# Kernel tuning notes

Hardware: AMD Instinct MI355X
Metric: run time of the kernel (lower is better)

## Reference

```python
import jax, jax.numpy as jnp
import numpy as np

T, B, DIM, N = 2048, 8, 1024, 64

def setup_inputs() -> dict:
    key = jax.random.key(0)
    ks = jax.random.split(key, 6)
    scale = 1.0 / np.sqrt(DIM)  # xavier-ish for Linear(dim, n_state)
    return {
        "x": jax.random.normal(ks[0], (T, B, DIM), dtype=jnp.float32),
        "S0": jnp.zeros((B, N, N), dtype=jnp.float32),
        "W_k": jax.random.normal(ks[1], (N, DIM), dtype=jnp.float32) * scale,
        "W_v": jax.random.normal(ks[2], (N, DIM), dtype=jnp.float32) * scale,
        "W_q": jax.random.normal(ks[3], (N, DIM), dtype=jnp.float32) * scale,
        "W_alpha": jax.random.normal(ks[4], (N, DIM), dtype=jnp.float32) * scale,
        "b_alpha": jnp.full((N,), 2.0, dtype=jnp.float32),
        "d_g": jnp.full((N,), 0.5, dtype=jnp.float32),
        "b_g": jnp.zeros((N,), dtype=jnp.float32),
    }

def reference(x, S0, W_k, W_v, W_q, W_alpha, b_alpha, d_g, b_g):
    # Precompute all projections: [T, B, N]
    k_all = jnp.einsum('tbd,nd->tbn', x, W_k)
    v_all = jnp.einsum('tbd,nd->tbn', x, W_v)
    q_all = jnp.einsum('tbd,nd->tbn', x, W_q)
    alpha_all = jax.nn.sigmoid(jnp.einsum('tbd,nd->tbn', x, W_alpha) + b_alpha)

    def step(S, inp):
        k, v, q, alpha = inp  # each [B, N]
        retrieved = jnp.einsum('bij,bj->bi', S, k)          # S @ k
        g = jax.nn.sigmoid(d_g * retrieved + b_g)
        v_gated = v * g
        outer_vk = jnp.einsum('bi,bj->bij', v_gated, k)
        S = alpha[..., None] * S + (1.0 - alpha[..., None]) * outer_vk
        out = jnp.einsum('bij,bj->bi', S, q)                # S @ q
        out = out * jax.nn.silu(out)                        # self-gate
        return S, out

    S_final, output = jax.lax.scan(step, S0, (k_all, v_all, q_all, alpha_all))
    return output, S_final
```

## Files before the change

### kernel.cpp

```cpp
#include <hip/hip_runtime.h>

#define TT 2048
#define BB 8
#define DD 1024
#define NN 64
#define C64 64
#define NC2 (TT / C64)

typedef __attribute__((ext_vector_type(8))) short bfrag;
typedef __attribute__((ext_vector_type(4))) float f32x4;
typedef __attribute__((ext_vector_type(8))) unsigned short ushort8;

__device__ __forceinline__ float rcp_(float x) { return __builtin_amdgcn_rcpf(x); }
__device__ __forceinline__ float exp2_(float x) {
#if __has_builtin(__builtin_amdgcn_exp2f)
    return __builtin_amdgcn_exp2f(x);
#else
    return exp2f(x);
#endif
}
__device__ __forceinline__ float sigmoidf_(float x) {
    return rcp_(1.0f + __expf(-x));
}
__device__ __forceinline__ float bcastlane(float x, int l) {
    return __int_as_float(__builtin_amdgcn_readlane(__float_as_int(x), l));
}

template <int CTRL, int RM>
__device__ __forceinline__ float dpp_mul1(float x) {
    int v = __builtin_amdgcn_update_dpp(
        0x3f800000, __float_as_int(x), CTRL, RM, 0xF, false);
    return x * __int_as_float(v);
}
__device__ __forceinline__ float prefix_mul64(float x) {
    x = dpp_mul1<0x111, 0xF>(x);
    x = dpp_mul1<0x112, 0xF>(x);
    x = dpp_mul1<0x114, 0xF>(x);
    x = dpp_mul1<0x118, 0xF>(x);
    x = dpp_mul1<0x142, 0xA>(x);
    x = dpp_mul1<0x143, 0xC>(x);
    return x;
}

__device__ __forceinline__ unsigned short cvt_bf16(float f) {
    unsigned int u = __float_as_uint(f);
    return (unsigned short)((u + 0x7FFF + ((u >> 16) & 1)) >> 16);
}

__device__ __forceinline__ void gll16(const float* g, float* l) {
    __builtin_amdgcn_global_load_lds(
        (const __attribute__((address_space(1))) void*)g,
        (__attribute__((address_space(3))) void*)l, 16, 0, 0);
}

__global__ __launch_bounds__(256) void wcvt_kernel(
    const float* __restrict__ W0, const float* __restrict__ W1,
    const float* __restrict__ W2, const float* __restrict__ W3,
    unsigned short* __restrict__ Wb)
{
    const int i = blockIdx.x * 256 + threadIdx.x;
    const int o = i * 8;
    const int col = o & 31;
    const int row = (o >> 5) & 63;
    const int kt  = (o >> 11) & 31;
    const int mat = o >> 16;
    const float* __restrict__ W = (mat == 0) ? W0 : (mat == 1) ? W1
                                 : (mat == 2) ? W2 : W3;
    const float* src = &W[(size_t)row * DD + kt * 32 + col];
    const float4 a = *(const float4*)src;
    const float4 b = *(const float4*)(src + 4);
    ushort8 r;
    r[0] = cvt_bf16(a.x); r[1] = cvt_bf16(a.y);
    r[2] = cvt_bf16(a.z); r[3] = cvt_bf16(a.w);
    r[4] = cvt_bf16(b.x); r[5] = cvt_bf16(b.y);
    r[6] = cvt_bf16(b.z); r[7] = cvt_bf16(b.w);
    *(ushort8*)&Wb[o] = r;
}

__global__ __launch_bounds__(256) void proj_fused_kernel(
    const float* __restrict__ x, const unsigned short* __restrict__ Wb,
    const float* __restrict__ b_alpha,
    float* __restrict__ O0, float* __restrict__ O1,
    float* __restrict__ O2, float* __restrict__ O3)
{
    const int m0   = blockIdx.x * 64;
    const int tid  = threadIdx.x;
    const int lane = tid & 63;
    const int wave = tid >> 6;
    const int ln   = lane & 15;
    const int q8   = (lane >> 4) * 8;

    __shared__ unsigned short As[64][40];
    __shared__ unsigned short Bs[4][64][40];

    f32x4 acc[4][4] = {};

    const int arow = tid >> 2;
    const int aseg = (tid & 3) * 8;

    float4 pa[2];
    ushort8 pw[4];
    {
        const float* ap = &x[(size_t)(m0 + arow) * DD + aseg];
        pa[0] = *(const float4*)ap;
        pa[1] = *(const float4*)(ap + 4);
        const ushort8* wp = (const ushort8*)&Wb[((size_t)(wave * 32 + 0) * 64 + lane) * 32];
        #pragma unroll
        for (int j = 0; j < 4; j++) pw[j] = wp[j];
    }

    for (int k0 = 0; k0 < DD; k0 += 32) {
        __syncthreads();
        {
            unsigned short t8[8];
            const float* pf = (const float*)pa;
            #pragma unroll
            for (int j = 0; j < 8; j++) t8[j] = cvt_bf16(pf[j]);
            *(ushort8*)&As[arow][aseg] = *(ushort8*)&t8[0];
            #pragma unroll
            for (int j = 0; j < 4; j++)
                *(ushort8*)&Bs[wave][lane][8 * j] = pw[j];
        }
        if (k0 + 32 < DD) {
            const int kt = (k0 >> 5) + 1;
            const float* ap = &x[(size_t)(m0 + arow) * DD + k0 + 32 + aseg];
            pa[0] = *(const float4*)ap;
            pa[1] = *(const float4*)(ap + 4);
            const ushort8* wp = (const ushort8*)&Wb[((size_t)(wave * 32 + kt) * 64 + lane) * 32];
            #pragma unroll
            for (int j = 0; j < 4; j++) pw[j] = wp[j];
        }
        __syncthreads();

        const bfrag af = *(const bfrag*)&As[wave * 16 + ln][q8];
        #pragma unroll
        for (int mat = 0; mat < 4; mat++) {
            bfrag bf[4];
            #pragma unroll
            for (int nt = 0; nt < 4; nt++)
                bf[nt] = *(const bfrag*)&Bs[mat][nt * 16 + ln][q8];
            #pragma unroll
            for (int nt = 0; nt < 4; nt++)
                acc[mat][nt] = __builtin_amdgcn_mfma_f32_16x16x32_bf16(
                    af, bf[nt], acc[mat][nt], 0, 0, 0);
        }
    }

    #pragma unroll
    for (int mat = 0; mat < 4; mat++) {
        float* __restrict__ C = (mat == 0) ? O0 : (mat == 1) ? O1
                               : (mat == 2) ? O2 : O3;
        #pragma unroll
        for (int nt = 0; nt < 4; nt++) {
            const int col = nt * 16 + ln;
            const float ba = (mat == 3) ? b_alpha[col] : 0.0f;
            #pragma unroll
            for (int r = 0; r < 4; r++) {
                const int row = m0 + wave * 16 + (lane >> 4) * 4 + r;
                float v = acc[mat][nt][r];
                if (mat == 3) v = sigmoidf_(v + ba);
                C[(size_t)row * NN + col] = v;
            }
        }
    }
}

__global__ __launch_bounds__(256) void gram_kernel(
    const float* __restrict__ k_all, const float* __restrict__ q_all,
    float* __restrict__ gkq)
{
    const int c  = blockIdx.x;
    const int b  = blockIdx.y;
    const int t0 = c * C64;
    const int tid = threadIdx.x;

    __shared__ __align__(16) float Ks[64][68];
    __shared__ __align__(16) float Qs[64][68];

    {
        const int r = tid >> 2, sg = (tid & 3) * 16;
        const float* kp = &k_all[(size_t)(t0 + r) * (BB * NN) + b * NN + sg];
        const float* qp = &q_all[(size_t)(t0 + r) * (BB * NN) + b * NN + sg];
        #pragma unroll
        for (int j = 0; j < 4; ++j) {
            *(float4*)&Ks[r][sg + 4 * j] = *(const float4*)(kp + 4 * j);
            *(float4*)&Qs[r][sg + 4 * j] = *(const float4*)(qp + 4 * j);
        }
    }
    __syncthreads();

    const int ti = tid >> 4, tj = tid & 15;
    float g[4][4] = {}, kq[4][4] = {};
    #pragma unroll
    for (int c4 = 0; c4 < 16; ++c4) {
        float4 ka[4], kb[4], qb[4];
        #pragma unroll
        for (int r = 0; r < 4; ++r) {
            ka[r] = *(const float4*)&Ks[4 * ti + r][c4 * 4];
            kb[r] = *(const float4*)&Ks[4 * tj + r][c4 * 4];
            qb[r] = *(const float4*)&Qs[4 * tj + r][c4 * 4];
        }
        #pragma unroll
        for (int r = 0; r < 4; ++r)
            #pragma unroll
            for (int q = 0; q < 4; ++q) {
                g[r][q]  = fmaf(ka[r].x, kb[q].x, g[r][q]);
                g[r][q]  = fmaf(ka[r].y, kb[q].y, g[r][q]);
                g[r][q]  = fmaf(ka[r].z, kb[q].z, g[r][q]);
                g[r][q]  = fmaf(ka[r].w, kb[q].w, g[r][q]);
                kq[r][q] = fmaf(ka[r].x, qb[q].x, kq[r][q]);
                kq[r][q] = fmaf(ka[r].y, qb[q].y, kq[r][q]);
                kq[r][q] = fmaf(ka[r].z, qb[q].z, kq[r][q]);
                kq[r][q] = fmaf(ka[r].w, qb[q].w, kq[r][q]);
            }
    }

    float* base = gkq + (size_t)(b * NC2 + c) * 64 * 128;
    #pragma unroll
    for (int r = 0; r < 4; ++r) {
        #pragma unroll
        for (int q = 0; q < 4; ++q) {
            const int t   = 4 * tj + q;
            const int pos = ((ti ^ (t & 15)) << 2) + r;
            base[t * 128 + pos]      = g[r][q];
            base[t * 128 + 64 + pos] = kq[r][q];
        }
    }
}

__global__ __launch_bounds__(128, 1) void scan_kernel(
    const float* __restrict__ gkq,
    const float* __restrict__ k_all, const float* __restrict__ q_all,
    const float* __restrict__ a_all, const float* __restrict__ v_all,
    const float* __restrict__ S0,
    const float* __restrict__ d_g, const float* __restrict__ b_g,
    float* __restrict__ out, float* __restrict__ S_final)
{
    const int b    = blockIdx.x;
    const int rg   = blockIdx.y;
    const int tid  = threadIdx.x;
    const int lane = tid & 63;
    const int wave = tid >> 6;
    const int row  = rg * 2 + wave;

    __shared__ __align__(16) float gT[2][64 * 128];
    __shared__ __align__(16) float Kl[2][64 * 64];
    __shared__ __align__(16) float Ql[2][64 * 64];
    __shared__ __align__(16) float sbuf[2][64];

    float S = S0[((size_t)b * NN + row) * NN + lane];
    const float L2E  = 1.4426950408889634f;
    const float ndg2 = -d_g[row] * L2E;
    const float nbg2 = -b_g[row] * L2E;

    const float* gkq_b = gkq + (size_t)b * NC2 * 64 * 128;

    const int s_loc = lane >> 4;
    const int gr    = lane & 15;

    auto stage = [&](int c, int db) {
        const float* src = gkq_b + (size_t)c * 64 * 128;
        #pragma unroll
        for (int j = 0; j < 16; ++j) {
            const int off = (wave * 32 + 2 * j) * 128;
            gll16(src + off + lane * 4, &gT[db][off]);
        }
        #pragma unroll
        for (int j = 0; j < 8; ++j) {
            const int r0 = wave * 32 + 4 * j;
            const int s  = r0 + s_loc;
            const int gg = gr ^ (s & 15);
            const size_t goff = ((size_t)(c * C64 + s) * BB + b) * NN + gg * 4;
            gll16(k_all + goff, &Kl[db][r0 * 64]);
            gll16(q_all + goff, &Ql[db][r0 * 64]);
        }
    };

    float a_nx, v_nx;
    auto aw_load = [&](int c) {
        const size_t goff = ((size_t)(c * C64 + lane) * BB + b) * NN + row;
        a_nx = a_all[goff];
        v_nx = v_all[goff];
    };

    stage(0, 0);
    aw_load(0);

    for (int c = 0; c < NC2; ++c) {
        const int db = c & 1;
        const float ac = a_nx;
        const float wc = (1.0f - a_nx) * v_nx;
        __syncthreads();
        if (c + 1 < NC2) { aw_load(c + 1); stage(c + 1, db ^ 1); }

        const float P  = prefix_mul64(ac);
        const float Pm = P / ac;
        const float u  = wc * rcp_(P);

        sbuf[wave][lane] = S;
        const float* Kb = &Kl[db][0];
        const float* Qb = &Ql[db][0];
        float4 ha = {0.f, 0.f, 0.f, 0.f};
        float4 hb = {0.f, 0.f, 0.f, 0.f};
        #pragma unroll
        for (int g4 = 0; g4 < 16; ++g4) {
            const int idx = lane * 64 + ((g4 ^ gr) << 2);
            float4 kv = *(const float4*)&Kb[idx];
            float4 qv = *(const float4*)&Qb[idx];
            float4 sv = *(const float4*)&sbuf[wave][g4 << 2];
            ha.x = fmaf(kv.x, sv.x, ha.x); ha.y = fmaf(kv.y, sv.y, ha.y);
            ha.z = fmaf(kv.z, sv.z, ha.z); ha.w = fmaf(kv.w, sv.w, ha.w);
            hb.x = fmaf(qv.x, sv.x, hb.x); hb.y = fmaf(qv.y, sv.y, hb.y);
            hb.z = fmaf(qv.z, sv.z, hb.z); hb.w = fmaf(qv.w, sv.w, hb.w);
        }
        const float h  = (ha.x + ha.y) + (ha.z + ha.w);
        const float hq = (hb.x + hb.y) + (hb.z + hb.w);
        const float e1 = ndg2 * Pm;
        const float e0 = fmaf(e1, h, nbg2);

        const float* gt = &gT[db][0];
        const int rowbase = lane * 128;

        float A = 0.f, Bacc = 0.f, Bl = 0.f, chl = 0.f;

        float4 ga0, ga1, qa0, qa1, gb0, gb1, qb0, qb1;

#define LOADBLK(G0, G1, Q0, Q1, blk) do {                                   \
        const int j0_ = ((2 * (blk)) ^ gr) << 2;                            \
        const int j1_ = ((2 * (blk) + 1) ^ gr) << 2;                        \
        G0 = *(const float4*)&gt[rowbase + j0_];                            \
        G1 = *(const float4*)&gt[rowbase + j1_];                            \
        Q0 = *(const float4*)&gt[rowbase + 64 + j0_];                       \
        Q1 = *(const float4*)&gt[rowbase + 64 + j1_];                       \
    } while (0)

#define STEP1(ss, gv, qv) do {                                              \
        const float sg_  = rcp_(1.0f + exp2_(fmaf(e1, A, e0)));             \
        const float s2_  = sg_ * u;                                         \
        const float chs_ = bcastlane(s2_, (ss));                            \
        A    = fmaf(chs_, (gv), A);                                         \
        Bacc = fmaf(chs_, (qv), Bacc);                                      \
        if (lane == (ss)) { Bl = Bacc; chl = chs_; }                        \
    } while (0)

#define STEP8(blk, G0, G1, Q0, Q1)                                          \
        STEP1(8 * (blk) + 0, G0.x, Q0.x); STEP1(8 * (blk) + 1, G0.y, Q0.y); \
        STEP1(8 * (blk) + 2, G0.z, Q0.z); STEP1(8 * (blk) + 3, G0.w, Q0.w); \
        STEP1(8 * (blk) + 4, G1.x, Q1.x); STEP1(8 * (blk) + 5, G1.y, Q1.y); \
        STEP1(8 * (blk) + 6, G1.z, Q1.z); STEP1(8 * (blk) + 7, G1.w, Q1.w);

        LOADBLK(ga0, ga1, qa0, qa1, 0);
        LOADBLK(gb0, gb1, qb0, qb1, 1);
        STEP8(0, ga0, ga1, qa0, qa1); LOADBLK(ga0, ga1, qa0, qa1, 2);
        STEP8(1, gb0, gb1, qb0, qb1); LOADBLK(gb0, gb1, qb0, qb1, 3);
        STEP8(2, ga0, ga1, qa0, qa1); LOADBLK(ga0, ga1, qa0, qa1, 4);
        STEP8(3, gb0, gb1, qb0, qb1); LOADBLK(gb0, gb1, qb0, qb1, 5);
        STEP8(4, ga0, ga1, qa0, qa1); LOADBLK(ga0, ga1, qa0, qa1, 6);
        STEP8(5, gb0, gb1, qb0, qb1); LOADBLK(gb0, gb1, qb0, qb1, 7);
        STEP8(6, ga0, ga1, qa0, qa1);
        STEP8(7, gb0, gb1, qb0, qb1);

#undef LOADBLK
#undef STEP1
#undef STEP8

        float Sa = 0.f;
        #pragma unroll
        for (int s = 0; s < 64; ++s) {
            const float chs = bcastlane(chl, s);
            const float kv  = Kb[s * 64 + (((lane >> 2) ^ (s & 15)) << 2) + (lane & 3)];
            Sa = fmaf(chs, kv, Sa);
        }

        const float o = P * (hq + Bl);
        const float y = o * o * rcp_(1.0f + exp2_(-o * L2E));
        out[((size_t)(c * C64 + lane) * BB + b) * NN + row] = y;
        const float Pl = bcastlane(P, 63);
        S = Pl * (S + Sa);
    }

    S_final[((size_t)b * NN + row) * NN + lane] = S;
}

extern "C" void kernel_launch(void* const* d_in, const int* in_sizes, int n_in,
                              void* d_out, int out_size, void* d_ws, size_t ws_size,
                              hipStream_t stream) {
    const float* x       = (const float*)d_in[0];
    const float* S0      = (const float*)d_in[1];
    const float* W_k     = (const float*)d_in[2];
    const float* W_v     = (const float*)d_in[3];
    const float* W_q     = (const float*)d_in[4];
    const float* W_alpha = (const float*)d_in[5];
    const float* b_alpha = (const float*)d_in[6];
    const float* d_g     = (const float*)d_in[7];
    const float* b_g     = (const float*)d_in[8];
    float* out = (float*)d_out;

    const size_t arr = (size_t)TT * BB * NN;
    float* ws    = (float*)d_ws;
    float* k_all = ws;
    float* v_all = ws + arr;
    float* q_all = ws + 2 * arr;
    float* a_all = ws + 3 * arr;
    float* gkq   = ws + 4 * arr;
    unsigned short* Wb = (unsigned short*)(ws + 6 * arr);

    wcvt_kernel<<<dim3(128), 256, 0, stream>>>(W_k, W_v, W_q, W_alpha, Wb);

    proj_fused_kernel<<<dim3(TT * BB / 64), 256, 0, stream>>>(
        x, Wb, b_alpha, k_all, v_all, q_all, a_all);

    gram_kernel<<<dim3(NC2, BB), 256, 0, stream>>>(k_all, q_all, gkq);

    scan_kernel<<<dim3(BB, 32), 128, 0, stream>>>(
        gkq, k_all, q_all, a_all, v_all, S0, d_g, b_g, out, out + arr);
}
```

Measured before the change: 319.9 us.

## Process four state rows per single-wave scan block with interleaved serial chains

```diff
diff --git a/kernel.cpp b/kernel.cpp
--- a/kernel.cpp
+++ b/kernel.cpp
@@ -228,7 +228,7 @@
     }
 }
 
-__global__ __launch_bounds__(128, 1) void scan_kernel(
+__global__ __launch_bounds__(64, 1) void scan_kernel(
     const float* __restrict__ gkq,
     const float* __restrict__ k_all, const float* __restrict__ q_all,
     const float* __restrict__ a_all, const float* __restrict__ v_all,
@@ -238,49 +238,52 @@
 {
     const int b    = blockIdx.x;
     const int rg   = blockIdx.y;
-    const int tid  = threadIdx.x;
-    const int lane = tid & 63;
-    const int wave = tid >> 6;
-    const int row  = rg * 2 + wave;
+    const int r0   = rg * 4;
+    const int lane = threadIdx.x;
+    const int gr    = lane & 15;
+    const int s_loc = lane >> 4;
 
     __shared__ __align__(16) float gT[2][64 * 128];
     __shared__ __align__(16) float Kl[2][64 * 64];
     __shared__ __align__(16) float Ql[2][64 * 64];
-    __shared__ __align__(16) float sbuf[2][64];
-
-    float S = S0[((size_t)b * NN + row) * NN + lane];
-    const float L2E  = 1.4426950408889634f;
-    const float ndg2 = -d_g[row] * L2E;
-    const float nbg2 = -b_g[row] * L2E;
+    __shared__ __align__(16) float sbuf[4][64];
+
+    const float L2E = 1.4426950408889634f;
+    const float4 dg4 = *(const float4*)&d_g[r0];
+    const float4 bg4 = *(const float4*)&b_g[r0];
+    float ndg2[4], nbg2[4], Sr[4];
+    #pragma unroll
+    for (int r = 0; r < 4; ++r) {
+        ndg2[r] = -((const float*)&dg4)[r] * L2E;
+        nbg2[r] = -((const float*)&bg4)[r] * L2E;
+        Sr[r]   = S0[((size_t)b * NN + r0 + r) * NN + lane];
+    }
 
     const float* gkq_b = gkq + (size_t)b * NC2 * 64 * 128;
-
-    const int s_loc = lane >> 4;
-    const int gr    = lane & 15;
 
     auto stage = [&](int c, int db) {
         const float* src = gkq_b + (size_t)c * 64 * 128;
         #pragma unroll
+        for (int j = 0; j < 32; ++j) {
+            const int off = (2 * j) * 128;
+            gll16(src + off + lane * 4, &gT[db][off]);
+        }
+        #pragma unroll
         for (int j = 0; j < 16; ++j) {
-            const int off = (wave * 32 + 2 * j) * 128;
-            gll16(src + off + lane * 4, &gT[db][off]);
-        }
-        #pragma unroll
-        for (int j = 0; j < 8; ++j) {
-            const int r0 = wave * 32 + 4 * j;
-            const int s  = r0 + s_loc;
+            const int rr = 4 * j;
+            const int s  = rr + s_loc;
             const int gg = gr ^ (s & 15);
             const size_t goff = ((size_t)(c * C64 + s) * BB + b) * NN + gg * 4;
-            gll16(k_all + goff, &Kl[db][r0 * 64]);
-            gll16(q_all + goff, &Ql[db][r0 * 64]);
+            gll16(k_all + goff, &Kl[db][rr * 64]);
+            gll16(q_all + goff, &Ql[db][rr * 64]);
         }
     };
 
-    float a_nx, v_nx;
+    float4 a_nx, v_nx;
     auto aw_load = [&](int c) {
-        const size_t goff = ((size_t)(c * C64 + lane) * BB + b) * NN + row;
-        a_nx = a_all[goff];
-        v_nx = v_all[goff];
+        const size_t goff = ((size_t)(c * C64 + lane) * BB + b) * NN + r0;
+        a_nx = *(const float4*)&a_all[goff];
+        v_nx = *(const float4*)&v_all[goff];
     };
 
     stage(0, 0);
@@ -288,66 +291,93 @@
 
     for (int c = 0; c < NC2; ++c) {
         const int db = c & 1;
-        const float ac = a_nx;
-        const float wc = (1.0f - a_nx) * v_nx;
+        float ac[4], wc[4];
+        #pragma unroll
+        for (int r = 0; r < 4; ++r) {
+            ac[r] = ((const float*)&a_nx)[r];
+            wc[r] = (1.0f - ac[r]) * ((const float*)&v_nx)[r];
+        }
         __syncthreads();
         if (c + 1 < NC2) { aw_load(c + 1); stage(c + 1, db ^ 1); }
 
-        const float P  = prefix_mul64(ac);
-        const float Pm = P / ac;
-        const float u  = wc * rcp_(P);
-
-        sbuf[wave][lane] = S;
+        float P[4], u[4], e1[4];
+        #pragma unroll
+        for (int r = 0; r < 4; ++r) {
+            P[r]  = prefix_mul64(ac[r]);
+            const float Pm = P[r] / ac[r];
+            u[r]  = wc[r] * rcp_(P[r]);
+            e1[r] = ndg2[r] * Pm;
+        }
+
+        #pragma unroll
+        for (int r = 0; r < 4; ++r) sbuf[r][lane] = Sr[r];
         const float* Kb = &Kl[db][0];
         const float* Qb = &Ql[db][0];
-        float4 ha = {0.f, 0.f, 0.f, 0.f};
-        float4 hb = {0.f, 0.f, 0.f, 0.f};
+        f32x4 hk[4] = {}, hqv[4] = {};
         #pragma unroll
         for (int g4 = 0; g4 < 16; ++g4) {
             const int idx = lane * 64 + ((g4 ^ gr) << 2);
-            float4 kv = *(const float4*)&Kb[idx];
-            float4 qv = *(const float4*)&Qb[idx];
-            float4 sv = *(const float4*)&sbuf[wave][g4 << 2];
-            ha.x = fmaf(kv.x, sv.x, ha.x); ha.y = fmaf(kv.y, sv.y, ha.y);
-            ha.z = fmaf(kv.z, sv.z, ha.z); ha.w = fmaf(kv.w, sv.w, ha.w);
-            hb.x = fmaf(qv.x, sv.x, hb.x); hb.y = fmaf(qv.y, sv.y, hb.y);
-            hb.z = fmaf(qv.z, sv.z, hb.z); hb.w = fmaf(qv.w, sv.w, hb.w);
-        }
-        const float h  = (ha.x + ha.y) + (ha.z + ha.w);
-        const float hq = (hb.x + hb.y) + (hb.z + hb.w);
-        const float e1 = ndg2 * Pm;
-        const float e0 = fmaf(e1, h, nbg2);
+            const f32x4 kv = *(const f32x4*)&Kb[idx];
+            const f32x4 qv = *(const f32x4*)&Qb[idx];
+            #pragma unroll
+            for (int r = 0; r < 4; ++r) {
+                const f32x4 sv = *(const f32x4*)&sbuf[r][g4 << 2];
+                hk[r][0] = fmaf(kv[0], sv[0], hk[r][0]);
+                hk[r][1] = fmaf(kv[1], sv[1], hk[r][1]);
+                hk[r][2] = fmaf(kv[2], sv[2], hk[r][2]);
+                hk[r][3] = fmaf(kv[3], sv[3], hk[r][3]);
+                hqv[r][0] = fmaf(qv[0], sv[0], hqv[r][0]);
+                hqv[r][1] = fmaf(qv[1], sv[1], hqv[r][1]);
+                hqv[r][2] = fmaf(qv[2], sv[2], hqv[r][2]);
+                hqv[r][3] = fmaf(qv[3], sv[3], hqv[r][3]);
+            }
+        }
+        float hq[4], z[4], Bacc[4], Bl[4], chl[4];
+        #pragma unroll
+        for (int r = 0; r < 4; ++r) {
+            const float h = (hk[r][0] + hk[r][1]) + (hk[r][2] + hk[r][3]);
+            hq[r] = (hqv[r][0] + hqv[r][1]) + (hqv[r][2] + hqv[r][3]);
+            z[r]  = fmaf(e1[r], h, nbg2[r]);
+            Bacc[r] = 0.f; Bl[r] = 0.f; chl[r] = 0.f;
+        }
 
         const float* gt = &gT[db][0];
         const int rowbase = lane * 128;
-
-        float A = 0.f, Bacc = 0.f, Bl = 0.f, chl = 0.f;
-
-        float4 ga0, ga1, qa0, qa1, gb0, gb1, qb0, qb1;
+        f32x4 ga0, ga1, qa0, qa1, gb0, gb1, qb0, qb1;
 
 #define LOADBLK(G0, G1, Q0, Q1, blk) do {                                   \
         const int j0_ = ((2 * (blk)) ^ gr) << 2;                            \
         const int j1_ = ((2 * (blk) + 1) ^ gr) << 2;                        \
-        G0 = *(const float4*)&gt[rowbase + j0_];                            \
-        G1 = *(const float4*)&gt[rowbase + j1_];                            \
-        Q0 = *(const float4*)&gt[rowbase + 64 + j0_];                       \
-        Q1 = *(const float4*)&gt[rowbase + 64 + j1_];                       \
+        G0 = *(const f32x4*)&gt[rowbase + j0_];                             \
+        G1 = *(const f32x4*)&gt[rowbase + j1_];                             \
+        Q0 = *(const f32x4*)&gt[rowbase + 64 + j0_];                        \
+        Q1 = *(const f32x4*)&gt[rowbase + 64 + j1_];                        \
     } while (0)
 
 #define STEP1(ss, gv, qv) do {                                              \
-        const float sg_  = rcp_(1.0f + exp2_(fmaf(e1, A, e0)));             \
-        const float s2_  = sg_ * u;                                         \
-        const float chs_ = bcastlane(s2_, (ss));                            \
-        A    = fmaf(chs_, (gv), A);                                         \
-        Bacc = fmaf(chs_, (qv), Bacc);                                      \
-        if (lane == (ss)) { Bl = Bacc; chl = chs_; }                        \
+        float zs_[4], sg_[4], ch_[4];                                       \
+        _Pragma("unroll")                                                   \
+        for (int r_ = 0; r_ < 4; ++r_) zs_[r_] = bcastlane(z[r_], (ss));    \
+        _Pragma("unroll")                                                   \
+        for (int r_ = 0; r_ < 4; ++r_)                                      \
+            sg_[r_] = rcp_(1.0f + exp2_(zs_[r_]));                          \
+        _Pragma("unroll")                                                   \
+        for (int r_ = 0; r_ < 4; ++r_)                                      \
+            ch_[r_] = sg_[r_] * bcastlane(u[r_], (ss));                     \
+        _Pragma("unroll")                                                   \
+        for (int r_ = 0; r_ < 4; ++r_) {                                    \
+            z[r_]    = fmaf((gv), ch_[r_] * e1[r_], z[r_]);                 \
+            Bacc[r_] = fmaf((qv), ch_[r_], Bacc[r_]);                       \
+            Bl[r_]   = (lane == (ss)) ? Bacc[r_] : Bl[r_];                  \
+            chl[r_]  = (lane == (ss)) ? ch_[r_]  : chl[r_];                 \
+        }                                                                   \
     } while (0)
 
 #define STEP8(blk, G0, G1, Q0, Q1)                                          \
-        STEP1(8 * (blk) + 0, G0.x, Q0.x); STEP1(8 * (blk) + 1, G0.y, Q0.y); \
-        STEP1(8 * (blk) + 2, G0.z, Q0.z); STEP1(8 * (blk) + 3, G0.w, Q0.w); \
-        STEP1(8 * (blk) + 4, G1.x, Q1.x); STEP1(8 * (blk) + 5, G1.y, Q1.y); \
-        STEP1(8 * (blk) + 6, G1.z, Q1.z); STEP1(8 * (blk) + 7, G1.w, Q1.w);
+        STEP1(8*(blk)+0, G0[0], Q0[0]); STEP1(8*(blk)+1, G0[1], Q0[1]);     \
+        STEP1(8*(blk)+2, G0[2], Q0[2]); STEP1(8*(blk)+3, G0[3], Q0[3]);     \
+        STEP1(8*(blk)+4, G1[0], Q1[0]); STEP1(8*(blk)+5, G1[1], Q1[1]);     \
+        STEP1(8*(blk)+6, G1[2], Q1[2]); STEP1(8*(blk)+7, G1[3], Q1[3]);
 
         LOADBLK(ga0, ga1, qa0, qa1, 0);
         LOADBLK(gb0, gb1, qb0, qb1, 1);
@@ -364,22 +394,29 @@
 #undef STEP1
 #undef STEP8
 
-        float Sa = 0.f;
+        float Sa[4] = {0.f, 0.f, 0.f, 0.f};
         #pragma unroll
         for (int s = 0; s < 64; ++s) {
-            const float chs = bcastlane(chl, s);
-            const float kv  = Kb[s * 64 + (((lane >> 2) ^ (s & 15)) << 2) + (lane & 3)];
-            Sa = fmaf(chs, kv, Sa);
-        }
-
-        const float o = P * (hq + Bl);
-        const float y = o * o * rcp_(1.0f + exp2_(-o * L2E));
-        out[((size_t)(c * C64 + lane) * BB + b) * NN + row] = y;
-        const float Pl = bcastlane(P, 63);
-        S = Pl * (S + Sa);
-    }
-
-    S_final[((size_t)b * NN + row) * NN + lane] = S;
+            const float kv = Kb[s * 64 +
+                ((((lane >> 2) << 2) ^ ((s & 15) << 2))) + (lane & 3)];
+            #pragma unroll
+            for (int r = 0; r < 4; ++r)
+                Sa[r] = fmaf(bcastlane(chl[r], s), kv, Sa[r]);
+        }
+
+        float4 y4;
+        #pragma unroll
+        for (int r = 0; r < 4; ++r) {
+            const float o = P[r] * (hq[r] + Bl[r]);
+            ((float*)&y4)[r] = o * o * rcp_(1.0f + exp2_(-o * L2E));
+            Sr[r] = bcastlane(P[r], 63) * (Sr[r] + Sa[r]);
+        }
+        *(float4*)&out[((size_t)(c * C64 + lane) * BB + b) * NN + r0] = y4;
+    }
+
+    #pragma unroll
+    for (int r = 0; r < 4; ++r)
+        S_final[((size_t)b * NN + r0 + r) * NN + lane] = Sr[r];
 }
 
 extern "C" void kernel_launch(void* const* d_in, const int* in_sizes, int n_in,
@@ -412,6 +449,6 @@
 
     gram_kernel<<<dim3(NC2, BB), 256, 0, stream>>>(k_all, q_all, gkq);
 
-    scan_kernel<<<dim3(BB, 32), 128, 0, stream>>>(
+    scan_kernel<<<dim3(BB, 16), 64, 0, stream>>>(
         gkq, k_all, q_all, a_all, v_all, S0, d_g, b_g, out, out + arr);
 }
```

Result: slower. 499.5 us (+56.1%).
